# Performance work log

Measured on AMD Instinct MI355X. Metric: run time of the kernel, lower is better.

Reference implementation:

```python
import jax, jax.numpy as jnp
import numpy as np

PDIM = 64
SK = 3
LK = 13

def setup_inputs() -> dict:
    key = jax.random.key(0)
    ks = jax.random.split(key, 6)
    B, C, H, W = 16, 128, 64, 64
    x = jax.random.normal(ks[0], (B, C, H, W), dtype=jnp.float32)
    lk_filter = jax.random.normal(ks[1], (PDIM, PDIM, LK, LK), dtype=jnp.float32) * 0.02
    w1 = jax.random.normal(ks[2], (PDIM // 2, PDIM), dtype=jnp.float32) * 0.1
    b1 = jax.random.normal(ks[3], (PDIM // 2,), dtype=jnp.float32) * 0.1
    w2 = jax.random.normal(ks[4], (PDIM * SK * SK, PDIM // 2), dtype=jnp.float32) * 0.1
    b2 = jax.random.normal(ks[5], (PDIM * SK * SK,), dtype=jnp.float32) * 0.1
    return {"x": x, "lk_filter": lk_filter, "w1": w1, "b1": b1, "w2": w2, "b2": b2}

def reference(x, lk_filter, w1, b1, w2, b2):
    B, C, H, W = x.shape
    x1, x2 = x[:, :PDIM], x[:, PDIM:]

    # dwc_proj: global avg pool -> 1x1 conv -> GELU -> 1x1 conv (per-sample 3x3 kernels)
    pooled = jnp.mean(x[:, :PDIM], axis=(2, 3))                     # [B, pdim]
    h = jax.nn.gelu(pooled @ w1.T + b1, approximate=False)          # [B, pdim//2]
    dyn = (h @ w2.T + b2).reshape(B, PDIM, SK * SK)                 # [B, pdim, 9]

    # dynamic depthwise 3x3 conv, per (batch, channel) kernel, padding=1
    pad = SK // 2
    xp = jnp.pad(x1, ((0, 0), (0, 0), (pad, pad), (pad, pad)))
    patches = jnp.stack([xp[:, :, i:i + H, j:j + W]
                         for i in range(SK) for j in range(SK)], axis=2)  # [B, pdim, 9, H, W]
    x1_dyn = jnp.einsum('bckhw,bck->bchw', patches, dyn)

    # large-kernel dense conv, padding = LK//2 (SAME for odd LK)
    p = LK // 2
    x1_lk = jax.lax.conv_general_dilated(
        x1, lk_filter, window_strides=(1, 1), padding=[(p, p), (p, p)],
        dimension_numbers=('NCHW', 'OIHW', 'NCHW'))

    x1_out = x1_lk + x1_dyn
    return jnp.concatenate([x1_out, x2], axis=1)
```

## Files before the change

### kernel.cpp

```cpp
#include <hip/hip_runtime.h>
#include <hip/hip_bf16.h>

typedef short  short8  __attribute__((ext_vector_type(8)));
typedef float  f32x16  __attribute__((ext_vector_type(16)));

#define XB 16
#define XC 128
#define XH 64
#define XW 64
#define XHW 4096
#define PSTR 72
#define XPROW 76

__device__ __forceinline__ unsigned short f2bf(float f) {
    union { float f; unsigned int u; } v; v.f = f;
    unsigned int r = (v.u + 0x7fffu + ((v.u >> 16) & 1u)) >> 16;
    return (unsigned short)r;
}

__global__ void k_prep(const float* __restrict__ x, unsigned short* __restrict__ xpad,
                       float* __restrict__ pooled,
                       const float* __restrict__ lk, unsigned short* __restrict__ fpack) {
    int blk = blockIdx.x;
    int t = threadIdx.x;
    if (blk >= 1216) {
        int tidx = (blk - 1216) * 256 + t;
        int l   = tidx & 63;
        int g   = (tidx >> 6) & 1;
        int ks  = (tidx >> 7) & 3;
        int tap = tidx >> 9;
        int oc  = g * 32 + (l & 31);
        int ic0 = ks * 16 + (l >> 5) * 8;
        unsigned short tmp[8];
#pragma unroll
        for (int e = 0; e < 8; ++e)
            tmp[e] = f2bf(lk[(size_t)(oc * 64 + ic0 + e) * 169 + tap]);
        unsigned int u[4];
#pragma unroll
        for (int k = 0; k < 4; ++k) u[k] = (unsigned int)tmp[2 * k] | ((unsigned int)tmp[2 * k + 1] << 16);
        uint4 v = {u[0], u[1], u[2], u[3]};
        *(uint4*)(fpack + (size_t)tidx * 8) = v;
        return;
    }
    int b = blk / 76, hp = blk - b * 76;
    unsigned short* dst = xpad + (size_t)(b * XPROW + hp) * XPROW * PSTR;
    uint4 z = {0u, 0u, 0u, 0u};
    if (hp < 6 || hp >= 70) {
        for (int k = t; k < 684; k += 256) ((uint4*)dst)[k] = z;
        return;
    }
    int h = hp - 6;
    __shared__ float tile[64][65];
    __shared__ float ps[4][64];
    {
        int w = t & 63, cg = t >> 6;
#pragma unroll
        for (int k = 0; k < 16; ++k) {
            int c = cg * 16 + k;
            tile[c][w] = x[(size_t)b * XC * XHW + (size_t)c * XHW + h * 64 + w];
        }
    }
    __syncthreads();
    {
        int c = t & 63, q = t >> 6;
        float s = 0.f;
#pragma unroll
        for (int k = 0; k < 16; ++k) s += tile[c][q * 16 + k];
        ps[q][c] = s;
    }
    __syncthreads();
    if (t < 64) {
        float tot = ps[0][t] + ps[1][t] + ps[2][t] + ps[3][t];
        atomicAdd(pooled + b * 64 + t, tot * (1.f / 4096.f));
    }
    if (t < 108) {
        int px = t / 9, u = t - (t / 9) * 9;
        int ppx = px < 6 ? px : px + 64;
        ((uint4*)(dst + ppx * PSTR))[u] = z;
    }
    {
        int px = t >> 2, cp = t & 3;
        unsigned short tmp[16];
#pragma unroll
        for (int k = 0; k < 16; ++k) tmp[k] = f2bf(tile[cp * 16 + k][px]);
        unsigned int u[8];
#pragma unroll
        for (int k = 0; k < 8; ++k) u[k] = (unsigned int)tmp[2 * k] | ((unsigned int)tmp[2 * k + 1] << 16);
        uint4 v0 = {u[0], u[1], u[2], u[3]};
        uint4 v1 = {u[4], u[5], u[6], u[7]};
        unsigned short* dp = dst + (px + 6) * PSTR + cp * 16;
        *(uint4*)dp = v0;
        *((uint4*)dp + 1) = v1;
        if (cp == 0) ((uint4*)(dst + (px + 6) * PSTR))[8] = z;
    }
}

#define LDSZ_H 112896
__global__ __launch_bounds__(512, 2) void k_conv(const unsigned short* __restrict__ xpad,
                                                 const unsigned short* __restrict__ fpack,
                                                 const float* __restrict__ pooled,
                                                 const float* __restrict__ w1, const float* __restrict__ b1,
                                                 const float* __restrict__ w2, const float* __restrict__ b2,
                                                 const float* __restrict__ x,
                                                 float* __restrict__ out) {
    extern __shared__ unsigned short lds[];
    unsigned short* ldsDyn = lds + 56448;
    float* ldsH = (float*)(lds + 57024);
    int blk = blockIdx.x;
    int b = blk >> 4, tile = blk & 15;
    int th = tile >> 2, tw = tile & 3;
    int Y0 = th * 16, X0 = tw * 16;
    int t = threadIdx.x;

    if (t < 32) {
        float s = b1[t];
        const float* pb = pooled + b * 64;
#pragma unroll
        for (int c = 0; c < 64; ++c) s += pb[c] * w1[t * 64 + c];
        ldsH[t] = 0.5f * s * (1.f + erff(s * 0.70710678118654752f));
    }

    {
        const unsigned short* srcb = xpad + ((size_t)(b * XPROW + Y0) * XPROW + X0) * PSTR;
        for (int k = t; k < 7056; k += 512) {
            int r = k / 252, o = k - r * 252;
            *(uint4*)(lds + r * 28 * PSTR + o * 8) =
                *(const uint4*)(srcb + (size_t)r * XPROW * PSTR + o * 8);
        }
    }
    __syncthreads();

    {
        float s = b2[t];
#pragma unroll
        for (int i = 0; i < 32; ++i) s += ldsH[i] * w2[t * 32 + i];
        ldsDyn[t] = f2bf(s);
        if (t < 64) {
            int o2 = 512 + t;
            float s2 = b2[o2];
#pragma unroll
            for (int i = 0; i < 32; ++i) s2 += ldsH[i] * w2[o2 * 32 + i];
            ldsDyn[o2] = f2bf(s2);
        }
    }
    __syncthreads();

    int wave = t >> 6, l = t & 63;
    int ks = wave & 3, fc = wave >> 2;
    int l31 = l & 31, lhi = l >> 5;

    int abase = ((l31 >> 3) * 28 + fc * 8 + (l31 & 7)) * PSTR + lhi * 8 + ks * 16;

    f32x16 acc[4][2];
#pragma unroll
    for (int m = 0; m < 4; ++m)
#pragma unroll
        for (int n = 0; n < 2; ++n)
#pragma unroll
            for (int r = 0; r < 16; ++r) acc[m][n][r] = 0.f;

    const unsigned short* fb = fpack + ks * 1024 + l * 8;

#pragma unroll 1
    for (int i = 0; i < 13; ++i) {
        const unsigned short* brow = fb + (size_t)(i * 13) * 4096;
        int arow = abase + i * 28 * PSTR;
#pragma unroll
        for (int j = 0; j < 13; ++j) {
            short8 b0 = *(const short8*)(brow + j * 4096);
            short8 b1v = *(const short8*)(brow + j * 4096 + 512);
            int aoff = arow + j * PSTR;
            __builtin_amdgcn_s_setprio(1);
#pragma unroll
            for (int fr = 0; fr < 4; ++fr) {
                short8 a = *(const short8*)(lds + aoff + fr * 8064);
                acc[fr][0] = __builtin_amdgcn_mfma_f32_32x32x16_bf16(a, b0, acc[fr][0], 0, 0, 0);
                acc[fr][1] = __builtin_amdgcn_mfma_f32_32x32x16_bf16(a, b1v, acc[fr][1], 0, 0, 0);
            }
            __builtin_amdgcn_s_setprio(0);
        }
    }

    {
        int ebase = ks * 16 + lhi * 8;
        int e0 = l31 - ebase;
        int e1 = 32 + l31 - ebase;
#pragma unroll
        for (int di = 0; di < 3; ++di)
#pragma unroll
            for (int dj = 0; dj < 3; ++dj) {
                int tp = di * 3 + dj;
                unsigned short v0 = ldsDyn[l31 * 9 + tp];
                unsigned short v1 = ldsDyn[(32 + l31) * 9 + tp];
                short8 b0, b1v;
#pragma unroll
                for (int s = 0; s < 8; ++s) {
                    b0[s] = (s == e0) ? (short)v0 : (short)0;
                    b1v[s] = (s == e1) ? (short)v1 : (short)0;
                }
                int aoff = abase + ((di + 5) * 28 + (dj + 5)) * PSTR;
#pragma unroll
                for (int fr = 0; fr < 4; ++fr) {
                    short8 a = *(const short8*)(lds + aoff + fr * 8064);
                    acc[fr][0] = __builtin_amdgcn_mfma_f32_32x32x16_bf16(a, b0, acc[fr][0], 0, 0, 0);
                    acc[fr][1] = __builtin_amdgcn_mfma_f32_32x32x16_bf16(a, b1v, acc[fr][1], 0, 0, 0);
                }
            }
    }
    __syncthreads();

    float* lf = (float*)lds;
#pragma unroll
    for (int fr = 0; fr < 4; ++fr) {
#pragma unroll
        for (int n = 0; n < 2; ++n)
#pragma unroll
            for (int r = 0; r < 16; ++r) {
                int oc = n * 32 + l31;
                int px = (r >> 2) * 16 + fc * 8 + (r & 3) + 4 * lhi;
                lf[ks * 4160 + oc * 65 + px] = acc[fr][n][r];
            }
        __syncthreads();
#pragma unroll
        for (int k2 = 0; k2 < 8; ++k2) {
            int e = k2 * 512 + t;
            int oc = e >> 6, px = e & 63;
            int idx = oc * 65 + px;
            float s = lf[idx] + lf[4160 + idx] + lf[8320 + idx] + lf[12480 + idx];
            int y = Y0 + fr * 4 + (px >> 4);
            int xx = X0 + (px & 15);
            out[((size_t)(b * XC + oc) * XH + y) * XW + xx] = s;
        }
        __syncthreads();
    }

    {
        const uint4* xs = (const uint4*)x;
        uint4* od = (uint4*)out;
#pragma unroll
        for (int q = 0; q < 8; ++q) {
            int m4 = blk * 4096 + q * 512 + t;
            int bi = m4 >> 16;
            int rem = m4 & 65535;
            size_t off = (size_t)bi * 131072 + 65536 + rem;
            od[off] = xs[off];
        }
    }
}

extern "C" void kernel_launch(void* const* d_in, const int* in_sizes, int n_in,
                              void* d_out, int out_size, void* d_ws, size_t ws_size,
                              hipStream_t stream) {
    const float* x  = (const float*)d_in[0];
    const float* lk = (const float*)d_in[1];
    const float* w1 = (const float*)d_in[2];
    const float* b1 = (const float*)d_in[3];
    const float* w2 = (const float*)d_in[4];
    const float* b2 = (const float*)d_in[5];
    float* out = (float*)d_out;

    char* ws = (char*)d_ws;
    float*          pooled = (float*)ws;
    unsigned short* fpack  = (unsigned short*)(ws + 40960);
    unsigned short* xpad   = (unsigned short*)(ws + 2605056);

    hipMemsetAsync(pooled, 0, 1024 * sizeof(float), stream);
    k_prep<<<1554, 256, 0, stream>>>(x, xpad, pooled, lk, fpack);
    k_conv<<<256, 512, 115328, stream>>>(xpad, fpack, pooled, w1, b1, w2, b2, x, out);
}
```

Measured before the change: 109.0 us.

## Stage filter taps through a double-buffered LDS ring with per-tap barriers

Instead of each wave loading its B filter fragments from global memory for every tap, the block now loads each tap's filter slice cooperatively once into a double-buffered LDS region. The next tap is prefetched from global while the current tap's MFMAs run. The 13x13 loops are flattened into one 169-step loop with a block-wide barrier per tap. This removes the duplicate global loads across the two fc wave groups, but adds 169 __syncthreads and raises dynamic LDS to 128 KiB.

```diff
diff --git a/kernel.cpp b/kernel.cpp
--- a/kernel.cpp
+++ b/kernel.cpp
@@ -95,7 +95,6 @@
     }
 }
 
-#define LDSZ_H 112896
 __global__ __launch_bounds__(512, 2) void k_conv(const unsigned short* __restrict__ xpad,
                                                  const unsigned short* __restrict__ fpack,
                                                  const float* __restrict__ pooled,
@@ -111,6 +110,7 @@
     int th = tile >> 2, tw = tile & 3;
     int Y0 = th * 16, X0 = tw * 16;
     int t = threadIdx.x;
+    int wave = t >> 6, l = t & 63;
 
     if (t < 32) {
         float s = b1[t];
@@ -128,6 +128,12 @@
                 *(const uint4*)(srcb + (size_t)r * XPROW * PSTR + o * 8);
         }
     }
+
+    const unsigned short* gB = fpack + wave * 512 + l * 8;
+    {
+        short8 b0s = *(const short8*)(gB);
+        *(short8*)(lds + 57344 + wave * 512 + l * 8) = b0s;
+    }
     __syncthreads();
 
     {
@@ -145,7 +151,6 @@
     }
     __syncthreads();
 
-    int wave = t >> 6, l = t & 63;
     int ks = wave & 3, fc = wave >> 2;
     int l31 = l & 31, lhi = l >> 5;
 
@@ -159,26 +164,29 @@
 #pragma unroll
             for (int r = 0; r < 16; ++r) acc[m][n][r] = 0.f;
 
-    const unsigned short* fb = fpack + ks * 1024 + l * 8;
-
+    int bbc = 57344;
+    int bread = bbc + ks * 1024 + l * 8;
+    const unsigned short* gBn = gB + 4096;
+    int ar = abase, jj = 0;
 #pragma unroll 1
-    for (int i = 0; i < 13; ++i) {
-        const unsigned short* brow = fb + (size_t)(i * 13) * 4096;
-        int arow = abase + i * 28 * PSTR;
-#pragma unroll
-        for (int j = 0; j < 13; ++j) {
-            short8 b0 = *(const short8*)(brow + j * 4096);
-            short8 b1v = *(const short8*)(brow + j * 4096 + 512);
-            int aoff = arow + j * PSTR;
-            __builtin_amdgcn_s_setprio(1);
-#pragma unroll
-            for (int fr = 0; fr < 4; ++fr) {
-                short8 a = *(const short8*)(lds + aoff + fr * 8064);
-                acc[fr][0] = __builtin_amdgcn_mfma_f32_32x32x16_bf16(a, b0, acc[fr][0], 0, 0, 0);
-                acc[fr][1] = __builtin_amdgcn_mfma_f32_32x32x16_bf16(a, b1v, acc[fr][1], 0, 0, 0);
-            }
-            __builtin_amdgcn_s_setprio(0);
-        }
+    for (int tt = 0; tt < 169; ++tt) {
+        short8 bnext = *(const short8*)(gBn);
+        gBn += 4096;
+        short8 b0 = *(const short8*)(lds + bread);
+        short8 b1v = *(const short8*)(lds + bread + 512);
+        __builtin_amdgcn_s_setprio(1);
+#pragma unroll
+        for (int fr = 0; fr < 4; ++fr) {
+            short8 a = *(const short8*)(lds + ar + fr * 8064);
+            acc[fr][0] = __builtin_amdgcn_mfma_f32_32x32x16_bf16(a, b0, acc[fr][0], 0, 0, 0);
+            acc[fr][1] = __builtin_amdgcn_mfma_f32_32x32x16_bf16(a, b1v, acc[fr][1], 0, 0, 0);
+        }
+        __builtin_amdgcn_s_setprio(0);
+        *(short8*)(lds + (bbc ^ 4096) + wave * 512 + l * 8) = bnext;
+        __syncthreads();
+        bbc ^= 4096; bread ^= 4096;
+        ++jj; ar += PSTR;
+        if (jj == 13) { jj = 0; ar += 15 * PSTR; }
     }
 
     {
@@ -266,5 +274,5 @@
 
     hipMemsetAsync(pooled, 0, 1024 * sizeof(float), stream);
     k_prep<<<1554, 256, 0, stream>>>(x, xpad, pooled, lk, fpack);
-    k_conv<<<256, 512, 115328, stream>>>(xpad, fpack, pooled, w1, b1, w2, b2, x, out);
-}
+    k_conv<<<256, 512, 131072, stream>>>(xpad, fpack, pooled, w1, b1, w2, b2, x, out);
+}
```

Result: no change. 110.8 us (+1.7%).
